# Kernel tuning notes

Hardware: AMD Instinct MI355X
Metric: run time of the kernel (lower is better)

## Reference

```python
import jax, jax.numpy as jnp
import numpy as np

N_TAGS = 256
SOS, EOS, PAD = 0, 1, 2
NEG = -1000000.0
B, T = 256, 512


def _init_transitions(key):
    t = jax.random.uniform(key, (N_TAGS, N_TAGS), jnp.float32, -0.1, 0.1)
    t = t.at[:, SOS].set(NEG)
    t = t.at[EOS, :].set(NEG)
    t = t.at[PAD, :].set(NEG)
    t = t.at[:, PAD].set(NEG)
    t = t.at[PAD, EOS].set(0.0)
    t = t.at[PAD, PAD].set(0.0)
    return t


def setup_inputs() -> dict:
    key = jax.random.key(0)
    k_em, k_tr = jax.random.split(key)
    emissions = jax.random.normal(k_em, (B, T, N_TAGS), jnp.float32)
    mask = jnp.ones((B, T), jnp.float32)
    transitions = _init_transitions(k_tr)
    return {"emissions": emissions, "mask": mask, "transitions": transitions}


def reference(emissions, mask, transitions):
    # Viterbi decode: max-plus DP over seq_len, then vectorized backtrace.
    # emissions: [B, T, n], mask: [B, T] float, transitions: [n, n]
    alphas0 = transitions[SOS][None, :] + emissions[:, 0]  # [B, n]
    em_rest = jnp.moveaxis(emissions[:, 1:], 1, 0)          # [T-1, B, n]
    m_rest = mask[:, 1:].T                                  # [T-1, B]

    def step(alphas, inp):
        em_t, m_t = inp
        # scores[b, prev, cur] = alphas[b, prev] + transitions[prev, cur] + em_t[b, cur]
        scores = alphas[:, :, None] + transitions[None, :, :] + em_t[:, None, :]
        max_scores = jnp.max(scores, axis=1)                 # [B, n]
        bpt = jnp.argmax(scores, axis=1).astype(jnp.int32)   # [B, n]
        new_alphas = m_t[:, None] * max_scores + (1.0 - m_t[:, None]) * alphas
        return new_alphas, bpt

    alphas, backptrs = jax.lax.scan(step, alphas0, (em_rest, m_rest))  # backptrs: [T-1, B, n]

    end_scores = alphas + transitions[:, EOS][None, :]       # [B, n]
    best_scores = jnp.max(end_scores, axis=1)                # [B]
    final_tags = jnp.argmax(end_scores, axis=1).astype(jnp.int32)  # [B]

    def back_step(tag, bpt):
        # tag: best tag at position t+1 ; bpt[b, tag] -> best tag at position t
        new_tag = jnp.take_along_axis(bpt, tag[:, None], axis=1)[:, 0]
        return new_tag, new_tag

    _, prev_tags = jax.lax.scan(back_step, final_tags, backptrs, reverse=True)
    # prev_tags: [T-1, B] in forward time order (tags for positions 0..T-2)
    paths = jnp.concatenate([prev_tags.T, final_tags[:, None]], axis=1)  # [B, T]
    return best_scores, paths
```

## Files before the change

kernel.cpp:

```cpp
#include <hip/hip_runtime.h>

#define NTAGS  256
#define TLEN   512
#define BATCH  256
#define HSPLIT 4
#define PP     64
#define NEGINF (-3.0e38f)

__global__ __launch_bounds__(1024, 4)
void viterbi_dp(const float* __restrict__ emis,
                const float* __restrict__ mask,
                const float* __restrict__ trans,
                float* __restrict__ out)
{
    __shared__ __align__(16) float alphaBuf[2][NTAGS];
    __shared__ __align__(16) float pval[HSPLIT][NTAGS];
    __shared__ __align__(16) int   parg[HSPLIT][NTAGS];
    __shared__ unsigned char bptL[(TLEN - 1) * NTAGS];
    __shared__ float endScore[NTAGS];

    const int tid = threadIdx.x;
    const int c = tid & (NTAGS - 1);
    const int h = tid >> 8;
    const int b = blockIdx.x;

    float treg[PP];
#pragma unroll
    for (int p = 0; p < PP; ++p)
        treg[p] = trans[(h * PP + p) * NTAGS + c];

    const float* eb = emis + (size_t)b * TLEN * NTAGS;
    const float* mb = mask + (size_t)b * TLEN;

    if (h == 0) alphaBuf[0][c] = trans[c] + eb[c];
    __syncthreads();

    float emCur = eb[NTAGS + c];
    float mCur  = mb[1];

    int cur = 0;
    for (int t = 1; t < TLEN; ++t) {
        float emNext = 0.0f, mNext = 1.0f;
        if (t + 1 < TLEN) {
            emNext = eb[(t + 1) * NTAGS + c];
            mNext  = mb[t + 1];
        }

        const float* alpha = alphaBuf[cur] + h * PP;
        float gb = NEGINF;
        int   ga = 0;
#pragma unroll
        for (int q = 0; q < PP / 4; ++q) {
            const float4 al = *(const float4*)(alpha + 4 * q);
            float s;
            s = (al.x + treg[4 * q + 0]) + emCur; if (s > gb) { gb = s; ga = 4 * q + 0; }
            s = (al.y + treg[4 * q + 1]) + emCur; if (s > gb) { gb = s; ga = 4 * q + 1; }
            s = (al.z + treg[4 * q + 2]) + emCur; if (s > gb) { gb = s; ga = 4 * q + 2; }
            s = (al.w + treg[4 * q + 3]) + emCur; if (s > gb) { gb = s; ga = 4 * q + 3; }
        }
        pval[h][c] = gb;
        parg[h][c] = ga;
        __syncthreads();

        if (h == 0) {
            float best = pval[0][c]; int arg = parg[0][c];
            float v1 = pval[1][c], v2 = pval[2][c], v3 = pval[3][c];
            if (v1 > best) { best = v1; arg =  64 + parg[1][c]; }
            if (v2 > best) { best = v2; arg = 128 + parg[2][c]; }
            if (v3 > best) { best = v3; arg = 192 + parg[3][c]; }
            const float aOld = alphaBuf[cur][c];
            alphaBuf[cur ^ 1][c] = mCur * best + (1.0f - mCur) * aOld;
            bptL[(t - 1) * NTAGS + c] = (unsigned char)arg;
        }
        emCur = emNext;
        mCur  = mNext;
        cur ^= 1;
        __syncthreads();
    }

    if (h == 0) endScore[c] = alphaBuf[cur][c] + trans[c * NTAGS + 1];
    __syncthreads();

    if (tid == 0) {
        float best = endScore[0]; int arg = 0;
        for (int i = 1; i < NTAGS; ++i) {
            float v = endScore[i];
            if (v > best) { best = v; arg = i; }
        }
        out[b] = best;

        float* pout = out + BATCH + (size_t)b * TLEN;
        int tag = arg;
        pout[TLEN - 1] = (float)tag;
        for (int t = TLEN - 2; t >= 0; --t) {
            tag = bptL[t * NTAGS + tag];
            pout[t] = (float)tag;
        }
    }
}

extern "C" void kernel_launch(void* const* d_in, const int* in_sizes, int n_in,
                              void* d_out, int out_size, void* d_ws, size_t ws_size,
                              hipStream_t stream) {
    (void)d_ws; (void)ws_size; (void)in_sizes; (void)n_in; (void)out_size;
    const float* emis  = (const float*)d_in[0];
    const float* mask  = (const float*)d_in[1];
    const float* trans = (const float*)d_in[2];
    float* out = (float*)d_out;

    viterbi_dp<<<dim3(BATCH), dim3(1024), 0, stream>>>(emis, mask, trans, out);
}
```

Before: 1.168 ms.

## Broadcast alphas via readlane and pack partial max/arg into float2

Each lane loads one alpha value from shared memory, and the 64 predecessor alphas are then broadcast across the wavefront with readlane into scalar registers, replacing the float4 LDS loads. Partial results from the other three quarters are packed into float2 {value, global index}, while quarter 0 keeps its own result in registers, so one fewer LDS write/read is needed. The alpha buffer becomes single-buffered because the second barrier separates reads from the update. The readlane sequence adds scalar-pipe work and SGPR pressure, and the register asm barrier constrains the compiler.

```diff
diff --git a/kernel.cpp b/kernel.cpp
--- a/kernel.cpp
+++ b/kernel.cpp
@@ -3,8 +3,6 @@
 #define NTAGS  256
 #define TLEN   512
 #define BATCH  256
-#define HSPLIT 4
-#define PP     64
 #define NEGINF (-3.0e38f)
 
 __global__ __launch_bounds__(1024, 4)
@@ -13,32 +11,34 @@
                 const float* __restrict__ trans,
                 float* __restrict__ out)
 {
-    __shared__ __align__(16) float alphaBuf[2][NTAGS];
-    __shared__ __align__(16) float pval[HSPLIT][NTAGS];
-    __shared__ __align__(16) int   parg[HSPLIT][NTAGS];
+    __shared__ __align__(16) float  alphaBuf[NTAGS];
+    __shared__ __align__(16) float2 pv[3][NTAGS];
     __shared__ unsigned char bptL[(TLEN - 1) * NTAGS];
     __shared__ float endScore[NTAGS];
 
-    const int tid = threadIdx.x;
-    const int c = tid & (NTAGS - 1);
-    const int h = tid >> 8;
-    const int b = blockIdx.x;
+    const int tid   = threadIdx.x;
+    const int c     = tid & (NTAGS - 1);
+    const int h     = tid >> 8;
+    const int lane  = tid & 63;
+    const int b     = blockIdx.x;
+    const int pbase = h * 64;
 
-    float treg[PP];
+    float treg[64];
 #pragma unroll
-    for (int p = 0; p < PP; ++p)
-        treg[p] = trans[(h * PP + p) * NTAGS + c];
+    for (int p = 0; p < 64; ++p) {
+        treg[p] = trans[(pbase + p) * NTAGS + c];
+        asm volatile("" : "+v"(treg[p]));
+    }
 
     const float* eb = emis + (size_t)b * TLEN * NTAGS;
     const float* mb = mask + (size_t)b * TLEN;
 
-    if (h == 0) alphaBuf[0][c] = trans[c] + eb[c];
+    if (h == 0) alphaBuf[c] = trans[c] + eb[c];
     __syncthreads();
 
     float emCur = eb[NTAGS + c];
     float mCur  = mb[1];
 
-    int cur = 0;
     for (int t = 1; t < TLEN; ++t) {
         float emNext = 0.0f, mNext = 1.0f;
         if (t + 1 < TLEN) {
@@ -46,39 +46,44 @@
             mNext  = mb[t + 1];
         }
 
-        const float* alpha = alphaBuf[cur] + h * PP;
+        const int avi = __float_as_int(alphaBuf[pbase + lane]);
+
         float gb = NEGINF;
         int   ga = 0;
 #pragma unroll
-        for (int q = 0; q < PP / 4; ++q) {
-            const float4 al = *(const float4*)(alpha + 4 * q);
+        for (int q = 0; q < 16; ++q) {
+            const float a0 = __int_as_float(__builtin_amdgcn_readlane(avi, 4 * q + 0));
+            const float a1 = __int_as_float(__builtin_amdgcn_readlane(avi, 4 * q + 1));
+            const float a2 = __int_as_float(__builtin_amdgcn_readlane(avi, 4 * q + 2));
+            const float a3 = __int_as_float(__builtin_amdgcn_readlane(avi, 4 * q + 3));
             float s;
-            s = (al.x + treg[4 * q + 0]) + emCur; if (s > gb) { gb = s; ga = 4 * q + 0; }
-            s = (al.y + treg[4 * q + 1]) + emCur; if (s > gb) { gb = s; ga = 4 * q + 1; }
-            s = (al.z + treg[4 * q + 2]) + emCur; if (s > gb) { gb = s; ga = 4 * q + 2; }
-            s = (al.w + treg[4 * q + 3]) + emCur; if (s > gb) { gb = s; ga = 4 * q + 3; }
+            s = (a0 + treg[4 * q + 0]) + emCur; if (s > gb) { gb = s; ga = 4 * q + 0; }
+            s = (a1 + treg[4 * q + 1]) + emCur; if (s > gb) { gb = s; ga = 4 * q + 1; }
+            s = (a2 + treg[4 * q + 2]) + emCur; if (s > gb) { gb = s; ga = 4 * q + 2; }
+            s = (a3 + treg[4 * q + 3]) + emCur; if (s > gb) { gb = s; ga = 4 * q + 3; }
         }
-        pval[h][c] = gb;
-        parg[h][c] = ga;
+
+        if (h) pv[h - 1][c] = make_float2(gb, __int_as_float(ga + pbase));
         __syncthreads();
 
         if (h == 0) {
-            float best = pval[0][c]; int arg = parg[0][c];
-            float v1 = pval[1][c], v2 = pval[2][c], v3 = pval[3][c];
-            if (v1 > best) { best = v1; arg =  64 + parg[1][c]; }
-            if (v2 > best) { best = v2; arg = 128 + parg[2][c]; }
-            if (v3 > best) { best = v3; arg = 192 + parg[3][c]; }
-            const float aOld = alphaBuf[cur][c];
-            alphaBuf[cur ^ 1][c] = mCur * best + (1.0f - mCur) * aOld;
+            const float2 P1 = pv[0][c];
+            const float2 P2 = pv[1][c];
+            const float2 P3 = pv[2][c];
+            float best = gb; int arg = ga;
+            if (P1.x > best) { best = P1.x; arg = __float_as_int(P1.y); }
+            if (P2.x > best) { best = P2.x; arg = __float_as_int(P2.y); }
+            if (P3.x > best) { best = P3.x; arg = __float_as_int(P3.y); }
+            const float aOld = alphaBuf[c];
+            alphaBuf[c] = mCur * best + (1.0f - mCur) * aOld;
             bptL[(t - 1) * NTAGS + c] = (unsigned char)arg;
         }
         emCur = emNext;
         mCur  = mNext;
-        cur ^= 1;
         __syncthreads();
     }
 
-    if (h == 0) endScore[c] = alphaBuf[cur][c] + trans[c * NTAGS + 1];
+    if (h == 0) endScore[c] = alphaBuf[c] + trans[c * NTAGS + 1];
     __syncthreads();
 
     if (tid == 0) {
```

New measurement: 1.534 ms. 31.3% more time.
